# Kernel tuning notes

Measured on AMD Instinct MI355X. Metric: run time of the kernel, lower is better.

Reference implementation:

```python
import jax, jax.numpy as jnp
import numpy as np

SPARSITY_RATIO = 0.9
K_CAP = 1024
Q_BLOCK = 256


def setup_inputs() -> dict:
    key = jax.random.key(0)
    k1, k2, k3 = jax.random.split(key, 3)
    BH, N, D = 32, 4096, 64
    q = jax.random.normal(k1, (BH, N, D), dtype=jnp.float32)
    k = jax.random.normal(k2, (BH, N, D), dtype=jnp.float32)
    v = jax.random.normal(k3, (BH, N, D), dtype=jnp.float32)
    return {"q": q, "k": k, "v": v}


def _streaming_topk_attention(q, k, v):
    # q,k,v: [BH, N, D]. Streaming block top-k sparse attention.
    BH, N, D = q.shape
    scale = 1.0 / np.sqrt(D)
    k_keep = min(max(1, int(N * (1.0 - SPARSITY_RATIO))), K_CAP)  # 409
    n_chunks = N // Q_BLOCK
    # [n_chunks, BH, qb, D] -- iterate q blocks to avoid full NxN scores
    q_chunks = q.reshape(BH, n_chunks, Q_BLOCK, D).transpose(1, 0, 2, 3)

    def chunk_fn(q_c):
        # scores for this q block vs all keys: [BH, qb, N]
        scores = jnp.einsum('bqd,bnd->bqn', q_c, k) * scale
        # running top-k over key blocks in the torch code == global top-k per row
        vals, idx = jax.lax.top_k(scores, k_keep)          # [BH, qb, k_keep]
        # stable softmax in fp32 over the kept scores (matches torch path)
        attn = jax.nn.softmax(vals.astype(jnp.float32), axis=-1).astype(q_c.dtype)
        # gather selected values: [BH, qb, k_keep, D]
        v_g = jax.vmap(lambda vv, ii: vv[ii])(v, idx)
        return jnp.einsum('bqk,bqkd->bqd', attn, v_g)       # [BH, qb, D]

    out = jax.lax.map(chunk_fn, q_chunks)                   # [n_chunks, BH, qb, D]
    return out.transpose(1, 0, 2, 3).reshape(BH, N, D)


def reference(q, k, v):
    return _streaming_topk_attention(q, k, v)
```

## Files before the change

### kernel.cpp

```cpp
#include <hip/hip_runtime.h>
#include <cstdint>
#include <cstddef>

#define BH_N    32
#define NK      4096
#define DIM     64
#define KKEEP   409
#define QSCALE  0.125f

#define MROWS   64
#define THREADS 512
#define CHUNK   128
#define NCHUNK  (NK / CHUNK)
#define HIST_LO 0.60f
#define HIST_INV 96.0f
#define HIST_BINS 192
#define EPS     0.005f
#define TH_GAP  (1.0f / HIST_INV + 4.0f * EPS)
#define CCAP    64

typedef _Float16 f16x8 __attribute__((ext_vector_type(8)));
typedef float f32x4 __attribute__((ext_vector_type(4)));

#define OFF_KC    0
#define OFF_VT    16384
#define OFF_PBUF  32768
#define OFF_HIST  16384
#define OFF_CANDJ 40960
#define OFF_MISC  49152
#define SMEM_SZ   (49152 + 7*256)

#define IMG_HALFS (CHUNK * DIM)
#define WS_NEED   ((size_t)2 * BH_N * NCHUNK * IMG_HALFS * sizeof(_Float16))

__device__ __forceinline__ int kc_off(int key, int g) {
  return key * 64 + ((g ^ (key & 7)) << 3);
}
__device__ __forceinline__ int vt_off(int d, int kb) {
  return d * 128 + ((kb ^ (d & 15) ^ (d >> 4)) << 3);
}
__device__ __forceinline__ int pb_off(int m, int g) {
  return m * 32 + ((g ^ (m & 3)) << 3);
}

typedef const __attribute__((address_space(1))) unsigned int gu32_t;
typedef __attribute__((address_space(3))) unsigned int lu32_t;
__device__ __forceinline__ void gload_lds16(const void* g, void* l) {
  __builtin_amdgcn_global_load_lds((gu32_t*)g, (lu32_t*)l, 16, 0, 0);
}

__global__ __launch_bounds__(512) void prep_images(
    const float* __restrict__ k, const float* __restrict__ v,
    _Float16* __restrict__ kimg, _Float16* __restrict__ vimg) {
  __shared__ float vstage[CHUNK * DIM];
  const int bid = blockIdx.x;
  const int t = threadIdx.x;
  const float* kb_ = k + (size_t)bid * CHUNK * DIM;
  const float* vb  = v + (size_t)bid * CHUNK * DIM;
  _Float16* ki = kimg + (size_t)bid * IMG_HALFS;
  _Float16* vi = vimg + (size_t)bid * IMG_HALFS;
#pragma unroll
  for (int s = 0; s < 4; ++s)
    ((float4*)vstage)[t + s * 512] = ((const float4*)vb)[t + s * 512];
#pragma unroll
  for (int s = 0; s < 2; ++s) {
    const int sid = t + s * 512, key = sid >> 3, g = sid & 7;
    const float* kr = kb_ + key * DIM + g * 8;
    float4 a0 = *(const float4*)kr, a1 = *(const float4*)(kr + 4);
    f16x8 h;
    h[0]=(_Float16)a0.x; h[1]=(_Float16)a0.y; h[2]=(_Float16)a0.z; h[3]=(_Float16)a0.w;
    h[4]=(_Float16)a1.x; h[5]=(_Float16)a1.y; h[6]=(_Float16)a1.z; h[7]=(_Float16)a1.w;
    *(f16x8*)(ki + kc_off(key, g)) = h;
  }
  __syncthreads();
#pragma unroll
  for (int s = 0; s < 2; ++s) {
    const int sid = t + s * 512, d = sid >> 4, kb = sid & 15;
    f16x8 h;
#pragma unroll
    for (int j = 0; j < 8; ++j) h[j] = (_Float16)vstage[(kb * 8 + j) * DIM + d];
    *(f16x8*)(vi + vt_off(d, kb)) = h;
  }
}

template <bool PRE>
__global__ __launch_bounds__(THREADS, 4) void fused_topk_attn(
    const float* __restrict__ q, const float* __restrict__ k,
    const float* __restrict__ v, float* __restrict__ out,
    const _Float16* __restrict__ kimg, const _Float16* __restrict__ vimg) {
  __shared__ __align__(16) unsigned char smem[SMEM_SZ];
  _Float16* kc   = (_Float16*)(smem + OFF_KC);
  _Float16* vt   = (_Float16*)(smem + OFF_VT);
  unsigned int* hist = (unsigned int*)(smem + OFF_HIST);
  _Float16* pbuf = (_Float16*)(smem + OFF_PBUF);
  unsigned short* candJ = (unsigned short*)(smem + OFF_CANDJ);
  int*   rmaxI  = (int*)(smem + OFF_MISC);
  float* thU    = (float*)(smem + OFF_MISC + 256);
  float* mval   = (float*)(smem + OFF_MISC + 768);
  unsigned int* candCnt = (unsigned int*)(smem + OFF_MISC + 1024);
  unsigned int* c1cnt   = (unsigned int*)(smem + OFF_MISC + 1280);
  float* zrow   = (float*)(smem + OFF_MISC + 1536);
  float* candS  = (float*)(smem + OFF_KC);
  float* outacc = (float*)(smem + OFF_VT);

  const int tid  = threadIdx.x;
  const int wave = tid >> 6, lane = tid & 63;
  const int am = lane & 15, aq = lane >> 4;
  const int mt = wave & 3, hh = wave >> 2;

  const int bid = blockIdx.x;
  const int xcd = bid & 7, idx = bid >> 3;
  const int bh  = xcd + 8 * (idx >> 6);
  const int mrow0 = (idx & 63) * MROWS;

  const float* qb = q + (size_t)bh * NK * DIM;
  const float* kb_ = k + (size_t)bh * NK * DIM;
  const float* vb = v + (size_t)bh * NK * DIM;
  float* ob = out + (size_t)bh * NK * DIM;

  for (int i = tid; i < 64 * (HIST_BINS / 2); i += THREADS) hist[i] = 0u;
  if (tid < 64) rmaxI[tid] = 0;
  __syncthreads();

  const int rbase = mrow0 + mt * 16;
  f16x8 A0, A1;
  {
    const float* qrow = qb + (size_t)(rbase + am) * DIM + aq * 8;
#pragma unroll
    for (int j = 0; j < 8; ++j) A0[j] = (_Float16)(qrow[j] * QSCALE);
#pragma unroll
    for (int j = 0; j < 8; ++j) A1[j] = (_Float16)(qrow[32 + j] * QSCALE);
  }

  float rmax[4] = {-1e30f, -1e30f, -1e30f, -1e30f};
#pragma unroll 1
  for (int ch = 0; ch < NCHUNK; ++ch) {
    const int key0 = ch * CHUNK;
    if constexpr (PRE) {
      const char* src = (const char*)(kimg + (size_t)(bh * NCHUNK + ch) * IMG_HALFS);
#pragma unroll
      for (int r = 0; r < 2; ++r)
        gload_lds16(src + r * 8192 + wave * 1024 + lane * 16,
                    smem + OFF_KC + r * 8192 + wave * 1024);
    } else {
      const int key = tid >> 2, seg = tid & 3;
      const float4* src = (const float4*)(kb_ + (size_t)(key0 + key) * DIM) + seg * 4;
      float4 a0 = src[0], a1 = src[1], a2 = src[2], a3 = src[3];
      f16x8 h0;
      h0[0]=(_Float16)a0.x; h0[1]=(_Float16)a0.y; h0[2]=(_Float16)a0.z; h0[3]=(_Float16)a0.w;
      h0[4]=(_Float16)a1.x; h0[5]=(_Float16)a1.y; h0[6]=(_Float16)a1.z; h0[7]=(_Float16)a1.w;
      *(f16x8*)(kc + kc_off(key, seg * 2)) = h0;
      f16x8 h1;
      h1[0]=(_Float16)a2.x; h1[1]=(_Float16)a2.y; h1[2]=(_Float16)a2.z; h1[3]=(_Float16)a2.w;
      h1[4]=(_Float16)a3.x; h1[5]=(_Float16)a3.y; h1[6]=(_Float16)a3.z; h1[7]=(_Float16)a3.w;
      *(f16x8*)(kc + kc_off(key, seg * 2 + 1)) = h1;
    }
    __syncthreads();
#pragma unroll
    for (int tl = 0; tl < 4; ++tl) {
      const int keyloc = hh * 64 + tl * 16 + am;
      f16x8 b0 = *(const f16x8*)(kc + kc_off(keyloc, aq));
      f16x8 b1 = *(const f16x8*)(kc + kc_off(keyloc, aq + 4));
      f32x4 acc = {0.f, 0.f, 0.f, 0.f};
      acc = __builtin_amdgcn_mfma_f32_16x16x32_f16(A0, b0, acc, 0, 0, 0);
      acc = __builtin_amdgcn_mfma_f32_16x16x32_f16(A1, b1, acc, 0, 0, 0);
#pragma unroll
      for (int r = 0; r < 4; ++r) {
        float s = acc[r];
        rmax[r] = fmaxf(rmax[r], s);
        if (s >= HIST_LO) {
          int bin = (int)((s - HIST_LO) * HIST_INV);
          bin = bin > (HIST_BINS - 1) ? (HIST_BINS - 1) : bin;
          atomicAdd(hist + (mt * 16 + aq * 4 + r) * (HIST_BINS / 2) + (bin >> 1),
                    (bin & 1) ? 65536u : 1u);
        }
      }
    }
    __syncthreads();
  }
#pragma unroll
  for (int off = 1; off < 16; off <<= 1)
#pragma unroll
    for (int r = 0; r < 4; ++r) rmax[r] = fmaxf(rmax[r], __shfl_xor(rmax[r], off));
  if (am == 0) {
#pragma unroll
    for (int r = 0; r < 4; ++r)
      atomicMax(rmaxI + mt * 16 + aq * 4 + r, __float_as_int(rmax[r]));
  }
  __syncthreads();

  if (tid < 64) {
    const unsigned int* hrow = hist + tid * (HIST_BINS / 2);
    unsigned int cum = 0; int bsel = 0;
    for (int b = HIST_BINS - 1; b >= 0; --b) {
      unsigned int pr = hrow[b >> 1];
      cum += (b & 1) ? (pr >> 16) : (pr & 0xffffu);
      if (cum >= KKEEP) { bsel = b; break; }
    }
    float lowerE = HIST_LO + (float)bsel * (1.0f / HIST_INV);
    float upperE = lowerE + (1.0f / HIST_INV);
    thU[tid] = upperE + 2.0f * EPS;
    mval[tid] = __int_as_float(rmaxI[tid]);
    candCnt[tid] = 0u; c1cnt[tid] = 0u; zrow[tid] = 0.f;
  }
  __syncthreads();

  float thU_r[4], m_r[4];
#pragma unroll
  for (int r = 0; r < 4; ++r) {
    int rb = mt * 16 + aq * 4 + r;
    thU_r[r] = thU[rb]; m_r[r] = mval[rb];
  }

  f32x4 pv[4];
#pragma unroll
  for (int d = 0; d < 4; ++d) pv[d] = (f32x4){0.f, 0.f, 0.f, 0.f};
  float zs[4] = {0.f, 0.f, 0.f, 0.f};
  int c1l[4] = {0, 0, 0, 0};
  _Float16* Pw = pbuf + wave * 512;

#pragma unroll 1
  for (int ch = 0; ch < NCHUNK; ++ch) {
    const int key0 = ch * CHUNK;
    if constexpr (PRE) {
      const char* ksrc = (const char*)(kimg + (size_t)(bh * NCHUNK + ch) * IMG_HALFS);
      const char* vsrc = (const char*)(vimg + (size_t)(bh * NCHUNK + ch) * IMG_HALFS);
#pragma unroll
      for (int r = 0; r < 2; ++r) {
        gload_lds16(ksrc + r * 8192 + wave * 1024 + lane * 16,
                    smem + OFF_KC + r * 8192 + wave * 1024);
        gload_lds16(vsrc + r * 8192 + wave * 1024 + lane * 16,
                    smem + OFF_VT + r * 8192 + wave * 1024);
      }
    } else {
      {
        const int key = tid >> 2, seg = tid & 3;
        const float4* src = (const float4*)(kb_ + (size_t)(key0 + key) * DIM) + seg * 4;
        float4 a0 = src[0], a1 = src[1], a2 = src[2], a3 = src[3];
        f16x8 h0;
        h0[0]=(_Float16)a0.x; h0[1]=(_Float16)a0.y; h0[2]=(_Float16)a0.z; h0[3]=(_Float16)a0.w;
        h0[4]=(_Float16)a1.x; h0[5]=(_Float16)a1.y; h0[6]=(_Float16)a1.z; h0[7]=(_Float16)a1.w;
        *(f16x8*)(kc + kc_off(key, seg * 2)) = h0;
        f16x8 h1;
        h1[0]=(_Float16)a2.x; h1[1]=(_Float16)a2.y; h1[2]=(_Float16)a2.z; h1[3]=(_Float16)a2.w;
        h1[4]=(_Float16)a3.x; h1[5]=(_Float16)a3.y; h1[6]=(_Float16)a3.z; h1[7]=(_Float16)a3.w;
        *(f16x8*)(kc + kc_off(key, seg * 2 + 1)) = h1;
      }
      {
        const int key = tid >> 2, seg = tid & 3;
        const float4* src = (const float4*)(vb + (size_t)(key0 + key) * DIM) + seg * 4;
        float4 a0 = src[0], a1 = src[1], a2 = src[2], a3 = src[3];
        const int kbg = key >> 3, kl = key & 7;
        const int d0 = seg * 16;
        vt[vt_off(d0 +  0, kbg) + kl] = (_Float16)a0.x;
        vt[vt_off(d0 +  1, kbg) + kl] = (_Float16)a0.y;
        vt[vt_off(d0 +  2, kbg) + kl] = (_Float16)a0.z;
        vt[vt_off(d0 +  3, kbg) + kl] = (_Float16)a0.w;
        vt[vt_off(d0 +  4, kbg) + kl] = (_Float16)a1.x;
        vt[vt_off(d0 +  5, kbg) + kl] = (_Float16)a1.y;
        vt[vt_off(d0 +  6, kbg) + kl] = (_Float16)a1.z;
        vt[vt_off(d0 +  7, kbg) + kl] = (_Float16)a1.w;
        vt[vt_off(d0 +  8, kbg) + kl] = (_Float16)a2.x;
        vt[vt_off(d0 +  9, kbg) + kl] = (_Float16)a2.y;
        vt[vt_off(d0 + 10, kbg) + kl] = (_Float16)a2.z;
        vt[vt_off(d0 + 11, kbg) + kl] = (_Float16)a2.w;
        vt[vt_off(d0 + 12, kbg) + kl] = (_Float16)a3.x;
        vt[vt_off(d0 + 13, kbg) + kl] = (_Float16)a3.y;
        vt[vt_off(d0 + 14, kbg) + kl] = (_Float16)a3.z;
        vt[vt_off(d0 + 15, kbg) + kl] = (_Float16)a3.w;
      }
    }
    __syncthreads();

#pragma unroll
    for (int grp = 0; grp < 2; ++grp) {
      *(f16x8*)(Pw + pb_off(am, aq)) = (f16x8){(_Float16)0,(_Float16)0,(_Float16)0,(_Float16)0,
                                               (_Float16)0,(_Float16)0,(_Float16)0,(_Float16)0};
#pragma unroll
      for (int t2 = 0; t2 < 2; ++t2) {
        const int keyloc = hh * 64 + grp * 32 + t2 * 16 + am;
        f16x8 b0 = *(const f16x8*)(kc + kc_off(keyloc, aq));
        f16x8 b1 = *(const f16x8*)(kc + kc_off(keyloc, aq + 4));
        f32x4 acc = {0.f, 0.f, 0.f, 0.f};
        acc = __builtin_amdgcn_mfma_f32_16x16x32_f16(A0, b0, acc, 0, 0, 0);
        acc = __builtin_amdgcn_mfma_f32_16x16x32_f16(A1, b1, acc, 0, 0, 0);
#pragma unroll
        for (int r = 0; r < 4; ++r) {
          float s = acc[r];
          if (s > thU_r[r]) {
            _Float16 wh = (_Float16)__expf(s - m_r[r]);
            zs[r] += (float)wh;
            c1l[r] += 1;
            const int m = aq * 4 + r, kl = t2 * 16 + am;
            Pw[m * 32 + (((kl >> 3) ^ (m & 3)) << 3) + (kl & 7)] = wh;
          } else if (s >= thU_r[r] - TH_GAP) {
            int rb = mt * 16 + aq * 4 + r;
            unsigned int p = atomicAdd(candCnt + rb, 1u);
            if (p < CCAP) candJ[rb * CCAP + p] = (unsigned short)(key0 + keyloc);
          }
        }
      }
      f16x8 pA = *(const f16x8*)(Pw + pb_off(am, aq));
#pragma unroll
      for (int dt = 0; dt < 4; ++dt) {
        f16x8 vB = *(const f16x8*)(vt + vt_off(dt * 16 + am, hh * 8 + grp * 4 + aq));
        pv[dt] = __builtin_amdgcn_mfma_f32_16x16x32_f16(pA, vB, pv[dt], 0, 0, 0);
      }
    }
    __syncthreads();
  }

  for (int i = tid; i < MROWS * DIM; i += THREADS) outacc[i] = 0.f;
  __syncthreads();
#pragma unroll
  for (int dt = 0; dt < 4; ++dt)
#pragma unroll
    for (int r = 0; r < 4; ++r)
      atomicAdd(outacc + (mt * 16 + aq * 4 + r) * 64 + dt * 16 + am, pv[dt][r]);
#pragma unroll
  for (int off = 1; off < 16; off <<= 1)
#pragma unroll
    for (int r = 0; r < 4; ++r) {
      zs[r] += __shfl_xor(zs[r], off);
      c1l[r] += __shfl_xor(c1l[r], off);
    }
  if (am == 0) {
#pragma unroll
    for (int r = 0; r < 4; ++r) {
      int rb = mt * 16 + aq * 4 + r;
      atomicAdd(zrow + rb, zs[r]);
      atomicAdd(c1cnt + rb, (unsigned int)c1l[r]);
    }
  }
  __syncthreads();

  unsigned short* wscr = (unsigned short*)(pbuf + wave * 512);
  const int cg = lane >> 3, le = lane & 7;
  for (int i = 0; i < 8; ++i) {
    const int rb = wave * 8 + i;
    const int nc = min((int)candCnt[rb], CCAP);
    int need = KKEEP - (int)c1cnt[rb];
    need = need < 0 ? 0 : (need > nc ? nc : need);
    const float mv = mval[rb];
    const float* qrow = qb + (size_t)(mrow0 + rb) * DIM + le * 8;
    float4 q0 = *(const float4*)qrow, q1 = *(const float4*)(qrow + 4);
    for (int base = 0; base < nc; base += 8) {
      const int c = base + cg;
      const bool act = c < nc;
      float p = 0.f;
      if (act) {
        int col = candJ[rb * CCAP + c] & (NK - 1);
        const float* kr = kb_ + (size_t)col * DIM + le * 8;
        float4 k0 = *(const float4*)kr, k1 = *(const float4*)(kr + 4);
        p = q0.x*k0.x + q0.y*k0.y + q0.z*k0.z + q0.w*k0.w
          + q1.x*k1.x + q1.y*k1.y + q1.z*k1.z + q1.w*k1.w;
        p *= QSCALE;
      }
      p += __shfl_xor(p, 1); p += __shfl_xor(p, 2); p += __shfl_xor(p, 4);
      if (act && le == 0) candS[rb * CCAP + c] = p;
    }
    float sc = (lane < nc) ? candS[rb * CCAP + lane] : -1e30f;
    int bi = __float_as_int(sc);
    unsigned int u = (bi >= 0) ? ((unsigned int)bi | 0x80000000u) : ~(unsigned int)bi;
    unsigned int T = 0;
    for (int bit = 31; bit >= 0; --bit) {
      unsigned int trial = T | (1u << bit);
      unsigned long long mk = __ballot((lane < nc) && (u >= trial));
      if (__popcll(mk) >= need) T = trial;
    }
    bool sel = (lane < nc) && (u > T);
    int need2 = need - __popcll(__ballot(sel));
    int col_l = (lane < nc) ? (int)(candJ[rb * CCAP + lane] & (NK - 1)) : 0x7fffffff;
    int guard = 0;
    while (need2 > 0 && guard < CCAP) {
      int cnd = (lane < nc && u == T && !sel) ? col_l : 0x7fffffff;
#pragma unroll
      for (int off = 1; off < 64; off <<= 1) cnd = min(cnd, __shfl_xor(cnd, off));
      if (lane < nc && u == T && col_l == cnd) sel = true;
      --need2; ++guard;
    }
    unsigned long long selm = __ballot(sel);
    const int scount = __popcll(selm);
    if (sel) {
      int slot = __popcll(selm & ((1ull << lane) - 1));
      wscr[slot] = (unsigned short)lane;
    }
    float po0 = 0.f, po1 = 0.f, po2 = 0.f, po3 = 0.f;
    float po4 = 0.f, po5 = 0.f, po6 = 0.f, po7 = 0.f;
    float zp = 0.f;
    for (int base = 0; base < scount; base += 8) {
      const int slot = base + cg;
      if (slot < scount) {
        const int c = wscr[slot];
        const float w = __expf(candS[rb * CCAP + c] - mv);
        const int col = candJ[rb * CCAP + c] & (NK - 1);
        const float* vr = vb + (size_t)col * DIM + le * 8;
        float4 v0 = *(const float4*)vr, v1 = *(const float4*)(vr + 4);
        po0 += w * v0.x; po1 += w * v0.y; po2 += w * v0.z; po3 += w * v0.w;
        po4 += w * v1.x; po5 += w * v1.y; po6 += w * v1.z; po7 += w * v1.w;
        zp += w;
      }
    }
#pragma unroll
    for (int off = 8; off < 64; off <<= 1) {
      po0 += __shfl_xor(po0, off); po1 += __shfl_xor(po1, off);
      po2 += __shfl_xor(po2, off); po3 += __shfl_xor(po3, off);
      po4 += __shfl_xor(po4, off); po5 += __shfl_xor(po5, off);
      po6 += __shfl_xor(po6, off); po7 += __shfl_xor(po7, off);
      zp  += __shfl_xor(zp,  off);
    }
    if (cg == 0) {
      float* orow = outacc + rb * 64 + le * 8;
      orow[0] += po0; orow[1] += po1; orow[2] += po2; orow[3] += po3;
      orow[4] += po4; orow[5] += po5; orow[6] += po6; orow[7] += po7;
      if (le == 0) zrow[rb] += zp;
    }
  }
  __syncthreads();

  for (int i = tid; i < MROWS * DIM; i += THREADS) {
    int rb = i >> 6;
    ob[(size_t)(mrow0 + rb) * DIM + (i & 63)] = outacc[i] / zrow[rb];
  }
}

extern "C" void kernel_launch(void* const* d_in, const int* in_sizes, int n_in,
                              void* d_out, int out_size, void* d_ws,
                              size_t ws_size, hipStream_t stream) {
  const float* q = (const float*)d_in[0];
  const float* k = (const float*)d_in[1];
  const float* v = (const float*)d_in[2];
  float* out = (float*)d_out;
  const int nblocks = (BH_N * NK) / MROWS;
  if (d_ws != nullptr && ws_size >= WS_NEED) {
    _Float16* kimg = (_Float16*)d_ws;
    _Float16* vimg = kimg + (size_t)BH_N * NCHUNK * IMG_HALFS;
    prep_images<<<BH_N * NCHUNK, 512, 0, stream>>>(k, v, kimg, vimg);
    fused_topk_attn<true><<<nblocks, THREADS, 0, stream>>>(q, k, v, out, kimg, vimg);
  } else {
    fused_topk_attn<false><<<nblocks, THREADS, 0, stream>>>(q, k, v, out, nullptr, nullptr);
  }
}
```

Before: 985.8 us.

## Double-buffer K chunk loads into LDS with async prefetch in both passes

Adds a second LDS buffer for K chunks so the next chunk's global_load_lds is issued while the current chunk is processed, replacing the per-chunk load/sync/compute/sync pattern with vmcnt waits and raw barriers. In the second pass V loads are issued first and waited on with vmcnt(2) after the first score group, so they overlap with score computation. LDS usage grows by 16 KB, which may reduce occupancy, and the hand-placed waitcnt and barrier ordering carries correctness risk. On the last iteration the prefetch wraps around to a redundant chunk 0 load.

```diff
diff --git a/kernel.cpp b/kernel.cpp
--- a/kernel.cpp
+++ b/kernel.cpp
@@ -22,13 +22,14 @@
 typedef _Float16 f16x8 __attribute__((ext_vector_type(8)));
 typedef float f32x4 __attribute__((ext_vector_type(4)));
 
-#define OFF_KC    0
-#define OFF_VT    16384
-#define OFF_PBUF  32768
-#define OFF_HIST  16384
-#define OFF_CANDJ 40960
-#define OFF_MISC  49152
-#define SMEM_SZ   (49152 + 7*256)
+#define OFF_KC0   0
+#define OFF_KC1   16384
+#define OFF_VT    32768
+#define OFF_HIST  32768
+#define OFF_PBUF  49152
+#define OFF_CANDJ 57344
+#define OFF_MISC  65536
+#define SMEM_SZ   (65536 + 7*256)
 
 #define IMG_HALFS (CHUNK * DIM)
 #define WS_NEED   ((size_t)2 * BH_N * NCHUNK * IMG_HALFS * sizeof(_Float16))
@@ -48,6 +49,9 @@
 __device__ __forceinline__ void gload_lds16(const void* g, void* l) {
   __builtin_amdgcn_global_load_lds((gu32_t*)g, (lu32_t*)l, 16, 0, 0);
 }
+#define VMCNT0() asm volatile("s_waitcnt vmcnt(0)" ::: "memory")
+#define VMCNT2() asm volatile("s_waitcnt vmcnt(2)" ::: "memory")
+#define RAWBAR() __builtin_amdgcn_s_barrier()
 
 __global__ __launch_bounds__(512) void prep_images(
     const float* __restrict__ k, const float* __restrict__ v,
@@ -89,7 +93,7 @@
     const float* __restrict__ v, float* __restrict__ out,
     const _Float16* __restrict__ kimg, const _Float16* __restrict__ vimg) {
   __shared__ __align__(16) unsigned char smem[SMEM_SZ];
-  _Float16* kc   = (_Float16*)(smem + OFF_KC);
+  _Float16* kc0  = (_Float16*)(smem + OFF_KC0);
   _Float16* vt   = (_Float16*)(smem + OFF_VT);
   unsigned int* hist = (unsigned int*)(smem + OFF_HIST);
   _Float16* pbuf = (_Float16*)(smem + OFF_PBUF);
@@ -100,7 +104,7 @@
   unsigned int* candCnt = (unsigned int*)(smem + OFF_MISC + 1024);
   unsigned int* c1cnt   = (unsigned int*)(smem + OFF_MISC + 1280);
   float* zrow   = (float*)(smem + OFF_MISC + 1536);
-  float* candS  = (float*)(smem + OFF_KC);
+  float* candS  = (float*)(smem + OFF_KC0);
   float* outacc = (float*)(smem + OFF_VT);
 
   const int tid  = threadIdx.x;
@@ -132,35 +136,49 @@
     for (int j = 0; j < 8; ++j) A1[j] = (_Float16)(qrow[32 + j] * QSCALE);
   }
 
+  const char* kimg_b = PRE ? (const char*)(kimg + (size_t)bh * NCHUNK * IMG_HALFS) : nullptr;
+  const char* vimg_b = PRE ? (const char*)(vimg + (size_t)bh * NCHUNK * IMG_HALFS) : nullptr;
+  const int soff = wave * 1024 + lane * 16;
+  const int doff = wave * 1024;
+
+  if constexpr (PRE) {
+#pragma unroll
+    for (int r = 0; r < 2; ++r)
+      gload_lds16(kimg_b + r * 8192 + soff, smem + OFF_KC0 + r * 8192 + doff);
+  }
   float rmax[4] = {-1e30f, -1e30f, -1e30f, -1e30f};
 #pragma unroll 1
   for (int ch = 0; ch < NCHUNK; ++ch) {
-    const int key0 = ch * CHUNK;
+    const _Float16* kcur;
     if constexpr (PRE) {
-      const char* src = (const char*)(kimg + (size_t)(bh * NCHUNK + ch) * IMG_HALFS);
+      VMCNT0();
+      RAWBAR();
+      const int nx = (ch + 1) & (NCHUNK - 1);
+      unsigned char* dst = smem + (((ch + 1) & 1) << 14);
 #pragma unroll
       for (int r = 0; r < 2; ++r)
-        gload_lds16(src + r * 8192 + wave * 1024 + lane * 16,
-                    smem + OFF_KC + r * 8192 + wave * 1024);
+        gload_lds16(kimg_b + (size_t)nx * 16384 + r * 8192 + soff, dst + r * 8192 + doff);
+      kcur = (const _Float16*)(smem + ((ch & 1) << 14));
     } else {
       const int key = tid >> 2, seg = tid & 3;
-      const float4* src = (const float4*)(kb_ + (size_t)(key0 + key) * DIM) + seg * 4;
+      const float4* src = (const float4*)(kb_ + (size_t)(ch * CHUNK + key) * DIM) + seg * 4;
       float4 a0 = src[0], a1 = src[1], a2 = src[2], a3 = src[3];
       f16x8 h0;
       h0[0]=(_Float16)a0.x; h0[1]=(_Float16)a0.y; h0[2]=(_Float16)a0.z; h0[3]=(_Float16)a0.w;
       h0[4]=(_Float16)a1.x; h0[5]=(_Float16)a1.y; h0[6]=(_Float16)a1.z; h0[7]=(_Float16)a1.w;
-      *(f16x8*)(kc + kc_off(key, seg * 2)) = h0;
+      *(f16x8*)(kc0 + kc_off(key, seg * 2)) = h0;
       f16x8 h1;
       h1[0]=(_Float16)a2.x; h1[1]=(_Float16)a2.y; h1[2]=(_Float16)a2.z; h1[3]=(_Float16)a2.w;
       h1[4]=(_Float16)a3.x; h1[5]=(_Float16)a3.y; h1[6]=(_Float16)a3.z; h1[7]=(_Float16)a3.w;
-      *(f16x8*)(kc + kc_off(key, seg * 2 + 1)) = h1;
-    }
-    __syncthreads();
+      *(f16x8*)(kc0 + kc_off(key, seg * 2 + 1)) = h1;
+      __syncthreads();
+      kcur = kc0;
+    }
 #pragma unroll
     for (int tl = 0; tl < 4; ++tl) {
       const int keyloc = hh * 64 + tl * 16 + am;
-      f16x8 b0 = *(const f16x8*)(kc + kc_off(keyloc, aq));
-      f16x8 b1 = *(const f16x8*)(kc + kc_off(keyloc, aq + 4));
+      f16x8 b0 = *(const f16x8*)(kcur + kc_off(keyloc, aq));
+      f16x8 b1 = *(const f16x8*)(kcur + kc_off(keyloc, aq + 4));
       f32x4 acc = {0.f, 0.f, 0.f, 0.f};
       acc = __builtin_amdgcn_mfma_f32_16x16x32_f16(A0, b0, acc, 0, 0, 0);
       acc = __builtin_amdgcn_mfma_f32_16x16x32_f16(A1, b1, acc, 0, 0, 0);
@@ -176,12 +194,13 @@
         }
       }
     }
-    __syncthreads();
+    if constexpr (!PRE) __syncthreads();
   }
 #pragma unroll
   for (int off = 1; off < 16; off <<= 1)
 #pragma unroll
     for (int r = 0; r < 4; ++r) rmax[r] = fmaxf(rmax[r], __shfl_xor(rmax[r], off));
+  __syncthreads();
   if (am == 0) {
 #pragma unroll
     for (int r = 0; r < 4; ++r)
@@ -222,16 +241,20 @@
 #pragma unroll 1
   for (int ch = 0; ch < NCHUNK; ++ch) {
     const int key0 = ch * CHUNK;
+    const _Float16* kcur;
     if constexpr (PRE) {
-      const char* ksrc = (const char*)(kimg + (size_t)(bh * NCHUNK + ch) * IMG_HALFS);
-      const char* vsrc = (const char*)(vimg + (size_t)(bh * NCHUNK + ch) * IMG_HALFS);
-#pragma unroll
-      for (int r = 0; r < 2; ++r) {
-        gload_lds16(ksrc + r * 8192 + wave * 1024 + lane * 16,
-                    smem + OFF_KC + r * 8192 + wave * 1024);
-        gload_lds16(vsrc + r * 8192 + wave * 1024 + lane * 16,
-                    smem + OFF_VT + r * 8192 + wave * 1024);
-      }
+      VMCNT0();
+      RAWBAR();
+#pragma unroll
+      for (int r = 0; r < 2; ++r)
+        gload_lds16(vimg_b + (size_t)ch * 16384 + r * 8192 + soff,
+                    smem + OFF_VT + r * 8192 + doff);
+      const int nx = (ch + 1) & (NCHUNK - 1);
+      unsigned char* dst = smem + (((ch + 1) & 1) << 14);
+#pragma unroll
+      for (int r = 0; r < 2; ++r)
+        gload_lds16(kimg_b + (size_t)nx * 16384 + r * 8192 + soff, dst + r * 8192 + doff);
+      kcur = (const _Float16*)(smem + ((ch & 1) << 14));
     } else {
       {
         const int key = tid >> 2, seg = tid & 3;
@@ -240,11 +263,11 @@
         f16x8 h0;
         h0[0]=(_Float16)a0.x; h0[1]=(_Float16)a0.y; h0[2]=(_Float16)a0.z; h0[3]=(_Float16)a0.w;
         h0[4]=(_Float16)a1.x; h0[5]=(_Float16)a1.y; h0[6]=(_Float16)a1.z; h0[7]=(_Float16)a1.w;
-        *(f16x8*)(kc + kc_off(key, seg * 2)) = h0;
+        *(f16x8*)(kc0 + kc_off(key, seg * 2)) = h0;
         f16x8 h1;
         h1[0]=(_Float16)a2.x; h1[1]=(_Float16)a2.y; h1[2]=(_Float16)a2.z; h1[3]=(_Float16)a2.w;
         h1[4]=(_Float16)a3.x; h1[5]=(_Float16)a3.y; h1[6]=(_Float16)a3.z; h1[7]=(_Float16)a3.w;
-        *(f16x8*)(kc + kc_off(key, seg * 2 + 1)) = h1;
+        *(f16x8*)(kc0 + kc_off(key, seg * 2 + 1)) = h1;
       }
       {
         const int key = tid >> 2, seg = tid & 3;
@@ -269,8 +292,9 @@
         vt[vt_off(d0 + 14, kbg) + kl] = (_Float16)a3.z;
         vt[vt_off(d0 + 15, kbg) + kl] = (_Float16)a3.w;
       }
-    }
-    __syncthreads();
+      __syncthreads();
+      kcur = kc0;
+    }
 
 #pragma unroll
     for (int grp = 0; grp < 2; ++grp) {
@@ -279,8 +303,8 @@
 #pragma unroll
       for (int t2 = 0; t2 < 2; ++t2) {
         const int keyloc = hh * 64 + grp * 32 + t2 * 16 + am;
-        f16x8 b0 = *(const f16x8*)(kc + kc_off(keyloc, aq));
-        f16x8 b1 = *(const f16x8*)(kc + kc_off(keyloc, aq + 4));
+        f16x8 b0 = *(const f16x8*)(kcur + kc_off(keyloc, aq));
+        f16x8 b1 = *(const f16x8*)(kcur + kc_off(keyloc, aq + 4));
         f32x4 acc = {0.f, 0.f, 0.f, 0.f};
         acc = __builtin_amdgcn_mfma_f32_16x16x32_f16(A0, b0, acc, 0, 0, 0);
         acc = __builtin_amdgcn_mfma_f32_16x16x32_f16(A1, b1, acc, 0, 0, 0);
@@ -300,6 +324,12 @@
           }
         }
       }
+      if constexpr (PRE) {
+        if (grp == 0) {
+          VMCNT2();
+          RAWBAR();
+        }
+      }
       f16x8 pA = *(const f16x8*)(Pw + pb_off(am, aq));
 #pragma unroll
       for (int dt = 0; dt < 4; ++dt) {
@@ -307,8 +337,9 @@
         pv[dt] = __builtin_amdgcn_mfma_f32_16x16x32_f16(pA, vB, pv[dt], 0, 0, 0);
       }
     }
-    __syncthreads();
-  }
+    if constexpr (!PRE) __syncthreads();
+  }
+  __syncthreads();
 
   for (int i = tid; i < MROWS * DIM; i += THREADS) outacc[i] = 0.f;
   __syncthreads();
```

Result: no change. 999.2 us (+1.4%).
